# Optimization experiments

Hardware: AMD Instinct MI355X
Metric: run time of the kernel (lower is better)

Reference implementation:

```python
import jax, jax.numpy as jnp
import numpy as np

BINS = 64
VMIN, VMAX = 0.0, 1.0
SIGMA = 0.02


def setup_inputs() -> dict:
    key = jax.random.key(0)
    x = jax.random.uniform(key, (8, 3, 512, 512), dtype=jnp.float32)
    centers = jnp.linspace(VMIN, VMAX, BINS, dtype=jnp.float32)
    return {"x": x, "centers": centers}


def reference(x, centers):
    B, C, H, W = x.shape
    xc = jnp.clip(x, VMIN, VMAX).reshape(B, C, H * W, 1)          # (B,C,P,1)
    c = centers.reshape(1, 1, 1, -1)                                # (1,1,1,bins)
    k = jnp.exp(-0.5 * ((xc - c) / (SIGMA + 1e-12)) ** 2)           # (B,C,P,bins)
    k = k / (jnp.sum(k, axis=-1, keepdims=True) + 1e-12)            # per-pixel normalize
    hist = jnp.mean(k, axis=2)                                      # (B,C,bins)
    hist = hist / (jnp.sum(hist, axis=-1, keepdims=True) + 1e-12)   # per-image normalize
    return hist
```

## Files before the change

kernel.cpp:

```cpp
#include <hip/hip_runtime.h>


#define NQ      1024
#define NBINS   64
#define NIMG    24
#define IMG_PIX (512 * 512)
#define BPI     32

__global__ __launch_bounds__(256) void soft_hist_table(
    const float* __restrict__ centers, float* __restrict__ table)
{
    const int t    = threadIdx.x;
    const int lane = t & 63;
    const int q    = blockIdx.x * 4 + (t >> 6);
    const float cq = ((float)q + 0.5f) * (1.0f / (float)NQ);
    const float d  = (cq - centers[lane]) * 50.0f;
    const float e  = expf(-0.5f * d * d);
    float s = e;
    #pragma unroll
    for (int off = 32; off > 0; off >>= 1) s += __shfl_xor(s, off, 64);
    table[q * NBINS + lane] = e / (s + 1e-12f);
}

__global__ __launch_bounds__(256) void soft_hist_count(
    const float* __restrict__ x, unsigned int* __restrict__ tot)
{
    __shared__ unsigned int h[NQ];
    const int t   = threadIdx.x;
    const int img = blockIdx.x;
    const int s   = blockIdx.y;

    #pragma unroll
    for (int k = 0; k < NQ / 256; ++k) h[t + k * 256] = 0u;
    __syncthreads();

    const float4* x4 = (const float4*)x
                     + (size_t)img * (IMG_PIX / 4)
                     + (size_t)s * (IMG_PIX / 4 / BPI);

    float4 v[8];
    #pragma unroll
    for (int r = 0; r < 8; ++r) v[r] = x4[r * 256 + t];

    #pragma unroll
    for (int r = 0; r < 8; ++r) {
        const float4 p = v[r];
        int q0 = (int)(p.x * (float)NQ); q0 = q0 < 0 ? 0 : (q0 > NQ - 1 ? NQ - 1 : q0);
        int q1 = (int)(p.y * (float)NQ); q1 = q1 < 0 ? 0 : (q1 > NQ - 1 ? NQ - 1 : q1);
        int q2 = (int)(p.z * (float)NQ); q2 = q2 < 0 ? 0 : (q2 > NQ - 1 ? NQ - 1 : q2);
        int q3 = (int)(p.w * (float)NQ); q3 = q3 < 0 ? 0 : (q3 > NQ - 1 ? NQ - 1 : q3);
        atomicAdd(&h[q0], 1u);
        atomicAdd(&h[q1], 1u);
        atomicAdd(&h[q2], 1u);
        atomicAdd(&h[q3], 1u);
    }
    __syncthreads();

    unsigned int* dst = tot + (size_t)img * NQ;
    #pragma unroll
    for (int k = 0; k < NQ / 256; ++k) {
        const int q = t + k * 256;
        const unsigned int c = h[q];
        if (c) atomicAdd(&dst[q], c);
    }
}

__global__ __launch_bounds__(256) void soft_hist_final(
    const unsigned int* __restrict__ tot, const float* __restrict__ table,
    float* __restrict__ out)
{
    __shared__ float tf[NQ];
    __shared__ float part[4][NBINS];
    const int t   = threadIdx.x;
    const int img = blockIdx.x;

    const unsigned int* src = tot + (size_t)img * NQ;
    #pragma unroll
    for (int k = 0; k < NQ / 256; ++k) tf[t + k * 256] = (float)src[t + k * 256];
    __syncthreads();

    const int j = t & 63;
    const int g = t >> 6;
    const int Q4 = NQ / 4;
    float acc = 0.0f;
    const float* tb = table + (size_t)(g * Q4) * NBINS + j;
    #pragma unroll 4
    for (int qq = 0; qq < Q4; ++qq)
        acc += tb[(size_t)qq * NBINS] * tf[g * Q4 + qq];
    part[g][j] = acc;
    __syncthreads();

    if (t < 64) {
        const float hsum = part[0][t] + part[1][t] + part[2][t] + part[3][t];
        const float hm   = hsum * (1.0f / (float)IMG_PIX);
        float ss = hm;
        #pragma unroll
        for (int off = 32; off > 0; off >>= 1) ss += __shfl_xor(ss, off, 64);
        out[img * NBINS + t] = hm / (ss + 1e-12f);
    }
}

extern "C" void kernel_launch(void* const* d_in, const int* in_sizes, int n_in,
                              void* d_out, int out_size, void* d_ws, size_t ws_size,
                              hipStream_t stream)
{
    const float* x       = (const float*)d_in[0];
    const float* centers = (const float*)d_in[1];
    float* out           = (float*)d_out;

    float*        table = (float*)d_ws;
    unsigned int* tot   = (unsigned int*)((char*)d_ws + (size_t)NQ * NBINS * sizeof(float));

    hipMemsetAsync(tot, 0, (size_t)NIMG * NQ * sizeof(unsigned int), stream);
    soft_hist_table<<<NQ / 4, 256, 0, stream>>>(centers, table);
    soft_hist_count<<<dim3(NIMG, BPI), 256, 0, stream>>>(x, tot);
    soft_hist_final<<<NIMG, 256, 0, stream>>>(tot, table, out);
}
```

Before: 91.21 us.

## Merge table and count kernels, replace global atomics with per-block partial histograms

Fuses the lookup-table kernel and the counting kernel into one launch whose extra blocks build the table. Each counting block now writes its own partial histogram instead of doing global atomics, so the memset is gone too. The final kernel sums the 32 partials per image before the matrix-vector product. This drops two launches or graph nodes and the global atomic contention. In exchange it adds about 3 MB of partial-histogram writes and reads, and serialises the reduction in a 24-block final kernel.

```diff
diff --git a/kernel.cpp b/kernel.cpp
--- a/kernel.cpp
+++ b/kernel.cpp
@@ -6,67 +6,60 @@
 #define NIMG    24
 #define IMG_PIX (512 * 512)
 #define BPI     32
+#define CNT_BLOCKS (NIMG * BPI)
+#define TBL_BLOCKS (NQ / 4)
 
-__global__ __launch_bounds__(256) void soft_hist_table(
-    const float* __restrict__ centers, float* __restrict__ table)
+__global__ __launch_bounds__(256) void soft_hist_k1(
+    const float* __restrict__ x, const float* __restrict__ centers,
+    float* __restrict__ table, unsigned int* __restrict__ parts)
 {
-    const int t    = threadIdx.x;
-    const int lane = t & 63;
-    const int q    = blockIdx.x * 4 + (t >> 6);
-    const float cq = ((float)q + 0.5f) * (1.0f / (float)NQ);
-    const float d  = (cq - centers[lane]) * 50.0f;
-    const float e  = expf(-0.5f * d * d);
-    float s = e;
-    #pragma unroll
-    for (int off = 32; off > 0; off >>= 1) s += __shfl_xor(s, off, 64);
-    table[q * NBINS + lane] = e / (s + 1e-12f);
-}
+    const int bid = blockIdx.x;
+    const int t   = threadIdx.x;
 
-__global__ __launch_bounds__(256) void soft_hist_count(
-    const float* __restrict__ x, unsigned int* __restrict__ tot)
-{
-    __shared__ unsigned int h[NQ];
-    const int t   = threadIdx.x;
-    const int img = blockIdx.x;
-    const int s   = blockIdx.y;
+    if (bid < CNT_BLOCKS) {
+        __shared__ unsigned int h[NQ];
+        #pragma unroll
+        for (int k = 0; k < NQ / 256; ++k) h[t + k * 256] = 0u;
+        __syncthreads();
 
-    #pragma unroll
-    for (int k = 0; k < NQ / 256; ++k) h[t + k * 256] = 0u;
-    __syncthreads();
+        const float4* x4 = (const float4*)x + (size_t)bid * (IMG_PIX / 4 / BPI);
 
-    const float4* x4 = (const float4*)x
-                     + (size_t)img * (IMG_PIX / 4)
-                     + (size_t)s * (IMG_PIX / 4 / BPI);
+        float4 v[8];
+        #pragma unroll
+        for (int r = 0; r < 8; ++r) v[r] = x4[r * 256 + t];
 
-    float4 v[8];
-    #pragma unroll
-    for (int r = 0; r < 8; ++r) v[r] = x4[r * 256 + t];
+        #pragma unroll
+        for (int r = 0; r < 8; ++r) {
+            const float4 p = v[r];
+            int q0 = (int)(p.x * (float)NQ); q0 = q0 < 0 ? 0 : (q0 > NQ - 1 ? NQ - 1 : q0);
+            int q1 = (int)(p.y * (float)NQ); q1 = q1 < 0 ? 0 : (q1 > NQ - 1 ? NQ - 1 : q1);
+            int q2 = (int)(p.z * (float)NQ); q2 = q2 < 0 ? 0 : (q2 > NQ - 1 ? NQ - 1 : q2);
+            int q3 = (int)(p.w * (float)NQ); q3 = q3 < 0 ? 0 : (q3 > NQ - 1 ? NQ - 1 : q3);
+            atomicAdd(&h[q0], 1u);
+            atomicAdd(&h[q1], 1u);
+            atomicAdd(&h[q2], 1u);
+            atomicAdd(&h[q3], 1u);
+        }
+        __syncthreads();
 
-    #pragma unroll
-    for (int r = 0; r < 8; ++r) {
-        const float4 p = v[r];
-        int q0 = (int)(p.x * (float)NQ); q0 = q0 < 0 ? 0 : (q0 > NQ - 1 ? NQ - 1 : q0);
-        int q1 = (int)(p.y * (float)NQ); q1 = q1 < 0 ? 0 : (q1 > NQ - 1 ? NQ - 1 : q1);
-        int q2 = (int)(p.z * (float)NQ); q2 = q2 < 0 ? 0 : (q2 > NQ - 1 ? NQ - 1 : q2);
-        int q3 = (int)(p.w * (float)NQ); q3 = q3 < 0 ? 0 : (q3 > NQ - 1 ? NQ - 1 : q3);
-        atomicAdd(&h[q0], 1u);
-        atomicAdd(&h[q1], 1u);
-        atomicAdd(&h[q2], 1u);
-        atomicAdd(&h[q3], 1u);
-    }
-    __syncthreads();
-
-    unsigned int* dst = tot + (size_t)img * NQ;
-    #pragma unroll
-    for (int k = 0; k < NQ / 256; ++k) {
-        const int q = t + k * 256;
-        const unsigned int c = h[q];
-        if (c) atomicAdd(&dst[q], c);
+        unsigned int* dst = parts + (size_t)bid * NQ;
+        #pragma unroll
+        for (int k = 0; k < NQ / 256; ++k) dst[t + k * 256] = h[t + k * 256];
+    } else {
+        const int lane = t & 63;
+        const int q    = (bid - CNT_BLOCKS) * 4 + (t >> 6);
+        const float cq = ((float)q + 0.5f) * (1.0f / (float)NQ);
+        const float d  = (cq - centers[lane]) * 50.0f;
+        const float e  = expf(-0.5f * d * d);
+        float s = e;
+        #pragma unroll
+        for (int off = 32; off > 0; off >>= 1) s += __shfl_xor(s, off, 64);
+        table[q * NBINS + lane] = e / (s + 1e-12f);
     }
 }
 
 __global__ __launch_bounds__(256) void soft_hist_final(
-    const unsigned int* __restrict__ tot, const float* __restrict__ table,
+    const unsigned int* __restrict__ parts, const float* __restrict__ table,
     float* __restrict__ out)
 {
     __shared__ float tf[NQ];
@@ -74,13 +67,19 @@
     const int t   = threadIdx.x;
     const int img = blockIdx.x;
 
-    const unsigned int* src = tot + (size_t)img * NQ;
+    const unsigned int* src = parts + (size_t)img * BPI * NQ;
     #pragma unroll
-    for (int k = 0; k < NQ / 256; ++k) tf[t + k * 256] = (float)src[t + k * 256];
+    for (int k = 0; k < NQ / 256; ++k) {
+        const int q = t + k * 256;
+        unsigned int s = 0;
+        #pragma unroll 8
+        for (int b = 0; b < BPI; ++b) s += src[(size_t)b * NQ + q];
+        tf[q] = (float)s;
+    }
     __syncthreads();
 
-    const int j = t & 63;
-    const int g = t >> 6;
+    const int j  = t & 63;
+    const int g  = t >> 6;
     const int Q4 = NQ / 4;
     float acc = 0.0f;
     const float* tb = table + (size_t)(g * Q4) * NBINS + j;
@@ -109,10 +108,9 @@
     float* out           = (float*)d_out;
 
     float*        table = (float*)d_ws;
-    unsigned int* tot   = (unsigned int*)((char*)d_ws + (size_t)NQ * NBINS * sizeof(float));
+    unsigned int* parts = (unsigned int*)((char*)d_ws
+                        + (size_t)NQ * NBINS * sizeof(float));
 
-    hipMemsetAsync(tot, 0, (size_t)NIMG * NQ * sizeof(unsigned int), stream);
-    soft_hist_table<<<NQ / 4, 256, 0, stream>>>(centers, table);
-    soft_hist_count<<<dim3(NIMG, BPI), 256, 0, stream>>>(x, tot);
-    soft_hist_final<<<NIMG, 256, 0, stream>>>(tot, table, out);
+    soft_hist_k1<<<CNT_BLOCKS + TBL_BLOCKS, 256, 0, stream>>>(x, centers, table, parts);
+    soft_hist_final<<<NIMG, 256, 0, stream>>>(parts, table, out);
 }
```

Measured after the change: 88.87 us. 1.03x faster.
